# Optimization experiments

Measured on AMD Instinct MI355X. Metric: run time of the kernel, lower is better.

Reference implementation:

```python
import jax, jax.numpy as jnp
import numpy as np

N_NODES = 100000
N_EDGES = 3200000
_EPS = 1e-6

# SE3 layout: [tx, ty, tz, qx, qy, qz, qw] (pypose convention)

def _normalize_se3(T):
    t, q = T[..., :3], T[..., 3:7]
    q = q / jnp.linalg.norm(q, axis=-1, keepdims=True)
    return jnp.concatenate([t, q], axis=-1)

def _qmul(q, r):
    qx, qy, qz, qw = q[..., 0], q[..., 1], q[..., 2], q[..., 3]
    rx, ry, rz, rw = r[..., 0], r[..., 1], r[..., 2], r[..., 3]
    x = qw * rx + qx * rw + qy * rz - qz * ry
    y = qw * ry - qx * rz + qy * rw + qz * rx
    z = qw * rz + qx * ry - qy * rx + qz * rw
    w = qw * rw - qx * rx - qy * ry - qz * rz
    return jnp.stack([x, y, z, w], axis=-1)

def _qrot(q, v):
    # rotate vector v by unit quaternion q: v + 2 w (u x v) + 2 u x (u x v)
    u, w = q[..., :3], q[..., 3:4]
    t = 2.0 * jnp.cross(u, v)
    return v + w * t + jnp.cross(u, t)

def _se3_inv(T):
    t, q = T[..., :3], T[..., 3:7]
    qc = q * jnp.asarray([-1.0, -1.0, -1.0, 1.0], dtype=T.dtype)
    ti = -_qrot(qc, t)
    return jnp.concatenate([ti, qc], axis=-1)

def _se3_mul(A, B):
    ta, qa = A[..., :3], A[..., 3:7]
    tb, qb = B[..., :3], B[..., 3:7]
    return jnp.concatenate([ta + _qrot(qa, tb), _qmul(qa, qb)], axis=-1)

def _so3_log(q):
    # quaternion (xyzw) -> axis-angle 3-vector
    v, w = q[..., :3], q[..., 3]
    n = jnp.linalg.norm(v, axis=-1)
    n_safe = jnp.where(n > _EPS, n, 1.0)
    scale = jnp.where(n > _EPS, 2.0 * jnp.arctan2(n, w) / n_safe, 2.0 / jnp.where(jnp.abs(w) > _EPS, w, 1.0))
    return v * scale[..., None]

def _se3_log(T):
    # SE3 -> se3 = [tau(3), phi(3)], tau = Jl(phi)^{-1} t
    t, q = T[..., :3], T[..., 3:7]
    phi = _so3_log(q)
    theta = jnp.linalg.norm(phi, axis=-1)
    small = theta < _EPS
    th = jnp.where(small, 1.0, theta)
    c = jnp.where(small, 1.0 / 12.0, 1.0 / th**2 - (1.0 + jnp.cos(th)) / (2.0 * th * jnp.sin(th)))
    pxt = jnp.cross(phi, t)
    tau = t - 0.5 * pxt + c[..., None] * jnp.cross(phi, pxt)
    return jnp.concatenate([tau, phi], axis=-1)

def setup_inputs() -> dict:
    key = jax.random.key(0)
    k1, k2, k3 = jax.random.split(key, 3)
    nodes = _normalize_se3(jax.random.normal(k1, (N_NODES, 7), dtype=jnp.float32))
    poses = _normalize_se3(jax.random.normal(k2, (N_EDGES, 7), dtype=jnp.float32))
    edges = jax.random.randint(k3, (N_EDGES, 2), 0, N_NODES, dtype=jnp.int64)
    return {"edges": edges, "poses": poses, "nodes": nodes}

def reference(edges, poses, nodes):
    node1 = nodes[edges[..., 0]]  # [E, 7]
    node2 = nodes[edges[..., 1]]  # [E, 7]
    error = _se3_mul(_se3_mul(_se3_inv(poses), node2), _se3_inv(node1))
    return _se3_log(error)  # [E, 6]
```

## Files before the change

### kernel.cpp

```cpp
#include <hip/hip_runtime.h>
#include <math.h>

#define BLOCK 256
#define EPS 1e-6f


struct F3 { float x, y, z; };
struct F4 { float x, y, z, w; };

__device__ __forceinline__ F3 cross3(F3 a, F3 b) {
    return F3{a.y * b.z - a.z * b.y,
              a.z * b.x - a.x * b.z,
              a.x * b.y - a.y * b.x};
}
__device__ __forceinline__ F3 add3(F3 a, F3 b) { return F3{a.x + b.x, a.y + b.y, a.z + b.z}; }
__device__ __forceinline__ F3 neg3(F3 a) { return F3{-a.x, -a.y, -a.z}; }

__device__ __forceinline__ F3 qrot(F4 q, F3 v) {
    F3 u{q.x, q.y, q.z};
    F3 t = cross3(u, v);
    t.x *= 2.0f; t.y *= 2.0f; t.z *= 2.0f;
    F3 c = cross3(u, t);
    return F3{v.x + q.w * t.x + c.x,
              v.y + q.w * t.y + c.y,
              v.z + q.w * t.z + c.z};
}
__device__ __forceinline__ F4 qmul(F4 q, F4 r) {
    return F4{
        q.w * r.x + q.x * r.w + q.y * r.z - q.z * r.y,
        q.w * r.y - q.x * r.z + q.y * r.w + q.z * r.x,
        q.w * r.z + q.x * r.y - q.y * r.x + q.z * r.w,
        q.w * r.w - q.x * r.x - q.y * r.y - q.z * r.z};
}

__device__ __forceinline__ void se3_error_log(
    F3 tp, F4 qp, F3 t1, F4 q1, F3 t2, F4 q2, float o[6])
{
    F4 qpc{-qp.x, -qp.y, -qp.z, qp.w};
    F3 tpi = neg3(qrot(qpc, tp));

    F3 tA = add3(tpi, qrot(qpc, t2));
    F4 qA = qmul(qpc, q2);

    F4 q1c{-q1.x, -q1.y, -q1.z, q1.w};
    F3 t1i = neg3(qrot(q1c, t1));

    F3 tE = add3(tA, qrot(qA, t1i));
    F4 qE = qmul(qA, q1c);

    F3 v{qE.x, qE.y, qE.z};
    float w = qE.w;
    float nn = sqrtf(v.x * v.x + v.y * v.y + v.z * v.z);

    float scale, c;
    if (nn > EPS) {
        float ang = 2.0f * atan2f(nn, w);
        float u = 1.0f / (ang * nn);
        scale = u * ang * ang;
        c = u * (u * nn * nn - 0.5f * w);
    } else {
        scale = 2.0f / ((fabsf(w) > EPS) ? w : 1.0f);
        c = 1.0f / 12.0f;
    }

    F3 phi{v.x * scale, v.y * scale, v.z * scale};
    F3 pxt = cross3(phi, tE);
    F3 ppxt = cross3(phi, pxt);
    o[0] = tE.x - 0.5f * pxt.x + c * ppxt.x;
    o[1] = tE.y - 0.5f * pxt.y + c * ppxt.y;
    o[2] = tE.z - 0.5f * pxt.z + c * ppxt.z;
    o[3] = phi.x; o[4] = phi.y; o[5] = phi.z;
}

__device__ __forceinline__ void gload_lds16(const void* g, void* lds) {
    __builtin_amdgcn_global_load_lds(
        (const __attribute__((address_space(1))) void*)g,
        (__attribute__((address_space(3))) void*)lds,
        16, 0, 0);
}

__global__ void __launch_bounds__(BLOCK) repack_nodes_kernel(
    const float* __restrict__ nodes, float* __restrict__ nodes8, int total7)
{
    int idx = blockIdx.x * BLOCK + threadIdx.x;
    int stride = gridDim.x * BLOCK;
    for (; idx < total7; idx += stride) {
        int node = idx / 7;
        int comp = idx - node * 7;
        nodes8[node * 8 + comp] = nodes[idx];
    }
}

__global__ void __launch_bounds__(BLOCK) pose_graph_kernel(
    const int* __restrict__ edges,
    const float* __restrict__ poses,
    const float* __restrict__ nodes8,
    float* __restrict__ out,
    int n)
{
    __shared__ float4 G[4][256];

    const int tid = threadIdx.x;
    const int l = tid & 63;
    const int w = tid >> 6;
    const long long base = (long long)blockIdx.x * BLOCK;
    const int limit = (int)min((long long)BLOCK, (long long)n - base);

    if (limit == BLOCK) {
        const long long e = base + tid;

        float pa[4], pb[4];
        {
            const char* pp = (const char*)poses + (size_t)e * 28;
            __builtin_memcpy(pa, pp, 16);
            __builtin_memcpy(pb, pp + 12, 16);
        }

        const int2 ed = ((const int2*)edges)[e];

#pragma unroll
        for (int k = 0; k < 4; ++k) {
            const int o = k * 16 + (l >> 2);
            const int m = (l & 3) ^ ((o >> 1) & 3);
            const int nx = __shfl(ed.x, o, 64);
            const int ny = __shfl(ed.y, o, 64);
            const int idx = (m & 2) ? ny : nx;
            gload_lds16((const char*)nodes8 + ((size_t)idx * 32 + (size_t)(m & 1) * 16),
                        &G[w][k * 64]);
        }

        asm volatile("s_waitcnt vmcnt(0)" ::: "memory");

        const int xo = (l >> 1) & 3;
        const int b4 = l * 4;
        float4 a1 = G[w][b4 + (0 ^ xo)];
        float4 b1 = G[w][b4 + (1 ^ xo)];
        float4 a2 = G[w][b4 + (2 ^ xo)];
        float4 b2 = G[w][b4 + (3 ^ xo)];

        F3 tp{pa[0], pa[1], pa[2]};
        F4 qp{pb[0], pb[1], pb[2], pb[3]};
        F3 t1{a1.x, a1.y, a1.z};
        F4 q1{a1.w, b1.x, b1.y, b1.z};
        F3 t2{a2.x, a2.y, a2.z};
        F4 q2{a2.w, b2.x, b2.y, b2.z};

        float o6[6];
        se3_error_log(tp, qp, t1, q1, t2, q2, o6);

        float* Gf = (float*)&G[w][0];
        Gf[l * 6 + 0] = o6[0];
        Gf[l * 6 + 1] = o6[1];
        Gf[l * 6 + 2] = o6[2];
        Gf[l * 6 + 3] = o6[3];
        Gf[l * 6 + 4] = o6[4];
        Gf[l * 6 + 5] = o6[5];
        asm volatile("s_waitcnt lgkmcnt(0)" ::: "memory");

        float4* odst = (float4*)(out + base * 6);
        odst[w * 96 + l] = G[w][l];
        if (l < 32)
            odst[w * 96 + 64 + l] = G[w][64 + l];
    } else {
        if (tid < limit) {
            const long long e = base + tid;
            const int2 ed = ((const int2*)edges)[e];
            const float* pp = poses + e * 7;
            F3 tp{pp[0], pp[1], pp[2]};
            F4 qp{pp[3], pp[4], pp[5], pp[6]};
            const float4* n1p = (const float4*)(nodes8 + (size_t)ed.x * 8);
            const float4* n2p = (const float4*)(nodes8 + (size_t)ed.y * 8);
            float4 a1 = n1p[0], b1 = n1p[1];
            float4 a2 = n2p[0], b2 = n2p[1];
            F3 t1{a1.x, a1.y, a1.z};
            F4 q1{a1.w, b1.x, b1.y, b1.z};
            F3 t2{a2.x, a2.y, a2.z};
            F4 q2{a2.w, b2.x, b2.y, b2.z};
            float o6[6];
            se3_error_log(tp, qp, t1, q1, t2, q2, o6);
            float* op = out + e * 6;
            op[0] = o6[0]; op[1] = o6[1]; op[2] = o6[2];
            op[3] = o6[3]; op[4] = o6[4]; op[5] = o6[5];
        }
    }
}

__global__ void __launch_bounds__(BLOCK) pose_graph_kernel_fallback(
    const int* __restrict__ edges, const float* __restrict__ poses,
    const float* __restrict__ nodes, float* __restrict__ out, int n)
{
    const int tid = threadIdx.x;
    const long long base = (long long)blockIdx.x * BLOCK;
    const int limit = (int)min((long long)BLOCK, (long long)n - base);
    if (tid < limit) {
        const long long e = base + tid;
        const int2 ed = ((const int2*)edges)[e];
        const float* pp = poses + e * 7;
        F3 tp{pp[0], pp[1], pp[2]};
        F4 qp{pp[3], pp[4], pp[5], pp[6]};
        const float* n1p = nodes + (size_t)ed.x * 7;
        const float* n2p = nodes + (size_t)ed.y * 7;
        F3 t1{n1p[0], n1p[1], n1p[2]};
        F4 q1{n1p[3], n1p[4], n1p[5], n1p[6]};
        F3 t2{n2p[0], n2p[1], n2p[2]};
        F4 q2{n2p[3], n2p[4], n2p[5], n2p[6]};
        float o6[6];
        se3_error_log(tp, qp, t1, q1, t2, q2, o6);
        float* op = out + e * 6;
        op[0] = o6[0]; op[1] = o6[1]; op[2] = o6[2];
        op[3] = o6[3]; op[4] = o6[4]; op[5] = o6[5];
    }
}

extern "C" void kernel_launch(void* const* d_in, const int* in_sizes, int n_in,
                              void* d_out, int out_size, void* d_ws, size_t ws_size,
                              hipStream_t stream) {
    const int* edges = (const int*)d_in[0];
    const float* poses = (const float*)d_in[1];
    const float* nodes = (const float*)d_in[2];
    float* out = (float*)d_out;

    const int n_edges = in_sizes[0] / 2;
    const int n_nodes = in_sizes[2] / 7;
    const int grid = (n_edges + BLOCK - 1) / BLOCK;

    const size_t ws_needed = (size_t)n_nodes * 8 * sizeof(float);
    if (ws_size >= ws_needed) {
        float* nodes8 = (float*)d_ws;
        const int total7 = n_nodes * 7;
        const int rgrid = (total7 + BLOCK - 1) / BLOCK;
        repack_nodes_kernel<<<rgrid, BLOCK, 0, stream>>>(nodes, nodes8, total7);
        pose_graph_kernel<<<grid, BLOCK, 0, stream>>>(edges, poses, nodes8, out, n_edges);
    } else {
        pose_graph_kernel_fallback<<<grid, BLOCK, 0, stream>>>(edges, poses, nodes, out, n_edges);
    }
}
```

Before: 217.5 us.

## Process four edge chunks per thread with software-pipelined direct node loads

```diff
diff --git a/kernel.cpp b/kernel.cpp
--- a/kernel.cpp
+++ b/kernel.cpp
@@ -2,6 +2,8 @@
 #include <math.h>
 
 #define BLOCK 256
+#define CPT 4
+#define TILE (BLOCK * CPT)
 #define EPS 1e-6f
 
 
@@ -72,13 +74,6 @@
     o[3] = phi.x; o[4] = phi.y; o[5] = phi.z;
 }
 
-__device__ __forceinline__ void gload_lds16(const void* g, void* lds) {
-    __builtin_amdgcn_global_load_lds(
-        (const __attribute__((address_space(1))) void*)g,
-        (__attribute__((address_space(3))) void*)lds,
-        16, 0, 0);
-}
-
 __global__ void __launch_bounds__(BLOCK) repack_nodes_kernel(
     const float* __restrict__ nodes, float* __restrict__ nodes8, int total7)
 {
@@ -91,6 +86,54 @@
     }
 }
 
+__device__ __forceinline__ void load_nodes(
+    const float* __restrict__ nodes8, int2 ed,
+    float4& a1, float4& b1, float4& a2, float4& b2)
+{
+    const float4* n1p = (const float4*)(nodes8 + (size_t)ed.x * 8);
+    const float4* n2p = (const float4*)(nodes8 + (size_t)ed.y * 8);
+    a1 = n1p[0]; b1 = n1p[1];
+    a2 = n2p[0]; b2 = n2p[1];
+}
+
+__device__ __forceinline__ void load_pose(
+    const float* __restrict__ poses, long long e, float pa[4], float pb[4])
+{
+    const char* pp = (const char*)poses + (size_t)e * 28;
+    __builtin_memcpy(pa, pp, 16);
+    __builtin_memcpy(pb, pp + 12, 16);
+}
+
+__device__ __forceinline__ void compute_store(
+    const float pa[4], const float pb[4],
+    float4 a1, float4 b1, float4 a2, float4 b2,
+    float* __restrict__ so,
+    const float4* __restrict__ SOw,
+    float4* __restrict__ odst_j,
+    int l)
+{
+    F3 tp{pa[0], pa[1], pa[2]};
+    F4 qp{pb[0], pb[1], pb[2], pb[3]};
+    F3 t1{a1.x, a1.y, a1.z};
+    F4 q1{a1.w, b1.x, b1.y, b1.z};
+    F3 t2{a2.x, a2.y, a2.z};
+    F4 q2{a2.w, b2.x, b2.y, b2.z};
+
+    float o6[6];
+    se3_error_log(tp, qp, t1, q1, t2, q2, o6);
+
+    so[l * 6 + 0] = o6[0];
+    so[l * 6 + 1] = o6[1];
+    so[l * 6 + 2] = o6[2];
+    so[l * 6 + 3] = o6[3];
+    so[l * 6 + 4] = o6[4];
+    so[l * 6 + 5] = o6[5];
+    asm volatile("s_waitcnt lgkmcnt(0)" ::: "memory");
+
+    odst_j[l] = SOw[l];
+    if (l < 32) odst_j[64 + l] = SOw[64 + l];
+}
+
 __global__ void __launch_bounds__(BLOCK) pose_graph_kernel(
     const int* __restrict__ edges,
     const float* __restrict__ poses,
@@ -98,89 +141,64 @@
     float* __restrict__ out,
     int n)
 {
-    __shared__ float4 G[4][256];
+    __shared__ float4 SO[4][96];
 
     const int tid = threadIdx.x;
     const int l = tid & 63;
     const int w = tid >> 6;
-    const long long base = (long long)blockIdx.x * BLOCK;
-    const int limit = (int)min((long long)BLOCK, (long long)n - base);
-
-    if (limit == BLOCK) {
-        const long long e = base + tid;
-
-        float pa[4], pb[4];
-        {
-            const char* pp = (const char*)poses + (size_t)e * 28;
-            __builtin_memcpy(pa, pp, 16);
-            __builtin_memcpy(pb, pp + 12, 16);
-        }
-
-        const int2 ed = ((const int2*)edges)[e];
-
-#pragma unroll
-        for (int k = 0; k < 4; ++k) {
-            const int o = k * 16 + (l >> 2);
-            const int m = (l & 3) ^ ((o >> 1) & 3);
-            const int nx = __shfl(ed.x, o, 64);
-            const int ny = __shfl(ed.y, o, 64);
-            const int idx = (m & 2) ? ny : nx;
-            gload_lds16((const char*)nodes8 + ((size_t)idx * 32 + (size_t)(m & 1) * 16),
-                        &G[w][k * 64]);
-        }
-
-        asm volatile("s_waitcnt vmcnt(0)" ::: "memory");
-
-        const int xo = (l >> 1) & 3;
-        const int b4 = l * 4;
-        float4 a1 = G[w][b4 + (0 ^ xo)];
-        float4 b1 = G[w][b4 + (1 ^ xo)];
-        float4 a2 = G[w][b4 + (2 ^ xo)];
-        float4 b2 = G[w][b4 + (3 ^ xo)];
-
-        F3 tp{pa[0], pa[1], pa[2]};
-        F4 qp{pb[0], pb[1], pb[2], pb[3]};
-        F3 t1{a1.x, a1.y, a1.z};
-        F4 q1{a1.w, b1.x, b1.y, b1.z};
-        F3 t2{a2.x, a2.y, a2.z};
-        F4 q2{a2.w, b2.x, b2.y, b2.z};
-
-        float o6[6];
-        se3_error_log(tp, qp, t1, q1, t2, q2, o6);
-
-        float* Gf = (float*)&G[w][0];
-        Gf[l * 6 + 0] = o6[0];
-        Gf[l * 6 + 1] = o6[1];
-        Gf[l * 6 + 2] = o6[2];
-        Gf[l * 6 + 3] = o6[3];
-        Gf[l * 6 + 4] = o6[4];
-        Gf[l * 6 + 5] = o6[5];
-        asm volatile("s_waitcnt lgkmcnt(0)" ::: "memory");
-
+    const long long base = (long long)blockIdx.x * TILE;
+
+    if (base + TILE <= (long long)n) {
+        const long long e0 = base + tid;
+
+        int2 ed0 = ((const int2*)edges)[e0];
+        int2 ed1 = ((const int2*)edges)[e0 + BLOCK];
+        int2 ed2 = ((const int2*)edges)[e0 + 2 * BLOCK];
+        int2 ed3 = ((const int2*)edges)[e0 + 3 * BLOCK];
+
+        float* so = (float*)&SO[w][0];
+        const float4* SOw = &SO[w][0];
         float4* odst = (float4*)(out + base * 6);
-        odst[w * 96 + l] = G[w][l];
-        if (l < 32)
-            odst[w * 96 + 64 + l] = G[w][64 + l];
+
+        float4 Aa, Ab, Ac, Ad; float Apa[4], Apb[4];
+        float4 Ba, Bb, Bc, Bd; float Bpa[4], Bpb[4];
+
+        load_nodes(nodes8, ed0, Aa, Ab, Ac, Ad);
+        load_pose(poses, e0, Apa, Apb);
+        load_nodes(nodes8, ed1, Ba, Bb, Bc, Bd);
+        load_pose(poses, e0 + BLOCK, Bpa, Bpb);
+
+        compute_store(Apa, Apb, Aa, Ab, Ac, Ad, so, SOw, odst + 0 * 384 + w * 96, l);
+        load_nodes(nodes8, ed2, Aa, Ab, Ac, Ad);
+        load_pose(poses, e0 + 2 * BLOCK, Apa, Apb);
+
+        compute_store(Bpa, Bpb, Ba, Bb, Bc, Bd, so, SOw, odst + 1 * 384 + w * 96, l);
+        load_nodes(nodes8, ed3, Ba, Bb, Bc, Bd);
+        load_pose(poses, e0 + 3 * BLOCK, Bpa, Bpb);
+
+        compute_store(Apa, Apb, Aa, Ab, Ac, Ad, so, SOw, odst + 2 * 384 + w * 96, l);
+        compute_store(Bpa, Bpb, Ba, Bb, Bc, Bd, so, SOw, odst + 3 * 384 + w * 96, l);
     } else {
-        if (tid < limit) {
-            const long long e = base + tid;
-            const int2 ed = ((const int2*)edges)[e];
-            const float* pp = poses + e * 7;
-            F3 tp{pp[0], pp[1], pp[2]};
-            F4 qp{pp[3], pp[4], pp[5], pp[6]};
-            const float4* n1p = (const float4*)(nodes8 + (size_t)ed.x * 8);
-            const float4* n2p = (const float4*)(nodes8 + (size_t)ed.y * 8);
-            float4 a1 = n1p[0], b1 = n1p[1];
-            float4 a2 = n2p[0], b2 = n2p[1];
-            F3 t1{a1.x, a1.y, a1.z};
-            F4 q1{a1.w, b1.x, b1.y, b1.z};
-            F3 t2{a2.x, a2.y, a2.z};
-            F4 q2{a2.w, b2.x, b2.y, b2.z};
-            float o6[6];
-            se3_error_log(tp, qp, t1, q1, t2, q2, o6);
-            float* op = out + e * 6;
-            op[0] = o6[0]; op[1] = o6[1]; op[2] = o6[2];
-            op[3] = o6[3]; op[4] = o6[4]; op[5] = o6[5];
+        for (int j = 0; j < CPT; ++j) {
+            const long long e = base + j * BLOCK + tid;
+            if (e < (long long)n) {
+                const int2 ed = ((const int2*)edges)[e];
+                float pa[4], pb[4];
+                load_pose(poses, e, pa, pb);
+                float4 a1, b1, a2, b2;
+                load_nodes(nodes8, ed, a1, b1, a2, b2);
+                F3 tp{pa[0], pa[1], pa[2]};
+                F4 qp{pb[0], pb[1], pb[2], pb[3]};
+                F3 t1{a1.x, a1.y, a1.z};
+                F4 q1{a1.w, b1.x, b1.y, b1.z};
+                F3 t2{a2.x, a2.y, a2.z};
+                F4 q2{a2.w, b2.x, b2.y, b2.z};
+                float o6[6];
+                se3_error_log(tp, qp, t1, q1, t2, q2, o6);
+                float* op = out + e * 6;
+                op[0] = o6[0]; op[1] = o6[1]; op[2] = o6[2];
+                op[3] = o6[3]; op[4] = o6[4]; op[5] = o6[5];
+            }
         }
     }
 }
@@ -222,16 +240,17 @@
 
     const int n_edges = in_sizes[0] / 2;
     const int n_nodes = in_sizes[2] / 7;
-    const int grid = (n_edges + BLOCK - 1) / BLOCK;
 
     const size_t ws_needed = (size_t)n_nodes * 8 * sizeof(float);
     if (ws_size >= ws_needed) {
         float* nodes8 = (float*)d_ws;
         const int total7 = n_nodes * 7;
         const int rgrid = (total7 + BLOCK - 1) / BLOCK;
+        const int grid = (n_edges + TILE - 1) / TILE;
         repack_nodes_kernel<<<rgrid, BLOCK, 0, stream>>>(nodes, nodes8, total7);
         pose_graph_kernel<<<grid, BLOCK, 0, stream>>>(edges, poses, nodes8, out, n_edges);
     } else {
+        const int grid = (n_edges + BLOCK - 1) / BLOCK;
         pose_graph_kernel_fallback<<<grid, BLOCK, 0, stream>>>(edges, poses, nodes, out, n_edges);
     }
 }
```

New measurement: 239.2 us. 1.1x slower.

## Process four edge chunks per block with double-buffered LDS gathers

Applied to the files above, without the earlier changes.

```diff
diff --git a/kernel.cpp b/kernel.cpp
--- a/kernel.cpp
+++ b/kernel.cpp
@@ -2,6 +2,8 @@
 #include <math.h>
 
 #define BLOCK 256
+#define CPT 4
+#define TILE (BLOCK * CPT)
 #define EPS 1e-6f
 
 
@@ -79,6 +81,65 @@
         16, 0, 0);
 }
 
+__device__ __forceinline__ void gather_wave(
+    const float* __restrict__ nodes8, int2 ed, int l, float4* __restrict__ GW)
+{
+#pragma unroll
+    for (int k = 0; k < 4; ++k) {
+        const int o = k * 16 + (l >> 2);
+        const int m = (l & 3) ^ ((o >> 1) & 3);
+        const int nx = __shfl(ed.x, o, 64);
+        const int ny = __shfl(ed.y, o, 64);
+        const int idx = (m & 2) ? ny : nx;
+        gload_lds16((const char*)nodes8 + ((size_t)idx * 32 + (size_t)(m & 1) * 16),
+                    GW + k * 64);
+    }
+}
+
+__device__ __forceinline__ void load_pose(
+    const float* __restrict__ poses, long long e, float pa[4], float pb[4])
+{
+    const char* pp = (const char*)poses + (size_t)e * 28;
+    __builtin_memcpy(pa, pp, 16);
+    __builtin_memcpy(pb, pp + 12, 16);
+}
+
+__device__ __forceinline__ void compute_store(
+    const float pa[4], const float pb[4],
+    float4* __restrict__ GW,
+    float4* __restrict__ odst_j,
+    int l)
+{
+    const int xo = (l >> 1) & 3;
+    const int b4 = l * 4;
+    float4 a1 = GW[b4 + (0 ^ xo)];
+    float4 b1 = GW[b4 + (1 ^ xo)];
+    float4 a2 = GW[b4 + (2 ^ xo)];
+    float4 b2 = GW[b4 + (3 ^ xo)];
+
+    F3 tp{pa[0], pa[1], pa[2]};
+    F4 qp{pb[0], pb[1], pb[2], pb[3]};
+    F3 t1{a1.x, a1.y, a1.z};
+    F4 q1{a1.w, b1.x, b1.y, b1.z};
+    F3 t2{a2.x, a2.y, a2.z};
+    F4 q2{a2.w, b2.x, b2.y, b2.z};
+
+    float o6[6];
+    se3_error_log(tp, qp, t1, q1, t2, q2, o6);
+
+    float* Gf = (float*)GW;
+    Gf[l * 6 + 0] = o6[0];
+    Gf[l * 6 + 1] = o6[1];
+    Gf[l * 6 + 2] = o6[2];
+    Gf[l * 6 + 3] = o6[3];
+    Gf[l * 6 + 4] = o6[4];
+    Gf[l * 6 + 5] = o6[5];
+    asm volatile("s_waitcnt lgkmcnt(0)" ::: "memory");
+
+    odst_j[l] = GW[l];
+    if (l < 32) odst_j[64 + l] = GW[64 + l];
+}
+
 __global__ void __launch_bounds__(BLOCK) repack_nodes_kernel(
     const float* __restrict__ nodes, float* __restrict__ nodes8, int total7)
 {
@@ -98,89 +159,74 @@
     float* __restrict__ out,
     int n)
 {
-    __shared__ float4 G[4][256];
+    __shared__ float4 G[4][2][256];
 
     const int tid = threadIdx.x;
     const int l = tid & 63;
     const int w = tid >> 6;
-    const long long base = (long long)blockIdx.x * BLOCK;
-    const int limit = (int)min((long long)BLOCK, (long long)n - base);
-
-    if (limit == BLOCK) {
-        const long long e = base + tid;
-
-        float pa[4], pb[4];
-        {
-            const char* pp = (const char*)poses + (size_t)e * 28;
-            __builtin_memcpy(pa, pp, 16);
-            __builtin_memcpy(pb, pp + 12, 16);
-        }
-
-        const int2 ed = ((const int2*)edges)[e];
-
-#pragma unroll
-        for (int k = 0; k < 4; ++k) {
-            const int o = k * 16 + (l >> 2);
-            const int m = (l & 3) ^ ((o >> 1) & 3);
-            const int nx = __shfl(ed.x, o, 64);
-            const int ny = __shfl(ed.y, o, 64);
-            const int idx = (m & 2) ? ny : nx;
-            gload_lds16((const char*)nodes8 + ((size_t)idx * 32 + (size_t)(m & 1) * 16),
-                        &G[w][k * 64]);
-        }
+    const long long base = (long long)blockIdx.x * TILE;
+
+    if (base + TILE <= (long long)n) {
+        const long long e0 = base + tid;
+
+        const int2 ed0 = ((const int2*)edges)[e0];
+        const int2 ed1 = ((const int2*)edges)[e0 + BLOCK];
+        const int2 ed2 = ((const int2*)edges)[e0 + 2 * BLOCK];
+        const int2 ed3 = ((const int2*)edges)[e0 + 3 * BLOCK];
+
+        float4* odst = (float4*)(out + base * 6);
+        float4* B0 = &G[w][0][0];
+        float4* B1 = &G[w][1][0];
+
+        float pa0[4], pb0[4], pa1[4], pb1[4];
+
+        gather_wave(nodes8, ed0, l, B0);
+        load_pose(poses, e0, pa0, pb0);
+
+        gather_wave(nodes8, ed1, l, B1);
+        load_pose(poses, e0 + BLOCK, pa1, pb1);
+        asm volatile("s_waitcnt vmcnt(8)" ::: "memory");
+        __builtin_amdgcn_sched_barrier(0);
+        compute_store(pa0, pb0, B0, odst + 0 * 384 + w * 96, l);
+
+        gather_wave(nodes8, ed2, l, B0);
+        load_pose(poses, e0 + 2 * BLOCK, pa0, pb0);
+        asm volatile("s_waitcnt vmcnt(8)" ::: "memory");
+        __builtin_amdgcn_sched_barrier(0);
+        compute_store(pa1, pb1, B1, odst + 1 * 384 + w * 96, l);
+
+        gather_wave(nodes8, ed3, l, B1);
+        load_pose(poses, e0 + 3 * BLOCK, pa1, pb1);
+        asm volatile("s_waitcnt vmcnt(8)" ::: "memory");
+        __builtin_amdgcn_sched_barrier(0);
+        compute_store(pa0, pb0, B0, odst + 2 * 384 + w * 96, l);
 
         asm volatile("s_waitcnt vmcnt(0)" ::: "memory");
-
-        const int xo = (l >> 1) & 3;
-        const int b4 = l * 4;
-        float4 a1 = G[w][b4 + (0 ^ xo)];
-        float4 b1 = G[w][b4 + (1 ^ xo)];
-        float4 a2 = G[w][b4 + (2 ^ xo)];
-        float4 b2 = G[w][b4 + (3 ^ xo)];
-
-        F3 tp{pa[0], pa[1], pa[2]};
-        F4 qp{pb[0], pb[1], pb[2], pb[3]};
-        F3 t1{a1.x, a1.y, a1.z};
-        F4 q1{a1.w, b1.x, b1.y, b1.z};
-        F3 t2{a2.x, a2.y, a2.z};
-        F4 q2{a2.w, b2.x, b2.y, b2.z};
-
-        float o6[6];
-        se3_error_log(tp, qp, t1, q1, t2, q2, o6);
-
-        float* Gf = (float*)&G[w][0];
-        Gf[l * 6 + 0] = o6[0];
-        Gf[l * 6 + 1] = o6[1];
-        Gf[l * 6 + 2] = o6[2];
-        Gf[l * 6 + 3] = o6[3];
-        Gf[l * 6 + 4] = o6[4];
-        Gf[l * 6 + 5] = o6[5];
-        asm volatile("s_waitcnt lgkmcnt(0)" ::: "memory");
-
-        float4* odst = (float4*)(out + base * 6);
-        odst[w * 96 + l] = G[w][l];
-        if (l < 32)
-            odst[w * 96 + 64 + l] = G[w][64 + l];
+        __builtin_amdgcn_sched_barrier(0);
+        compute_store(pa1, pb1, B1, odst + 3 * 384 + w * 96, l);
     } else {
-        if (tid < limit) {
-            const long long e = base + tid;
-            const int2 ed = ((const int2*)edges)[e];
-            const float* pp = poses + e * 7;
-            F3 tp{pp[0], pp[1], pp[2]};
-            F4 qp{pp[3], pp[4], pp[5], pp[6]};
-            const float4* n1p = (const float4*)(nodes8 + (size_t)ed.x * 8);
-            const float4* n2p = (const float4*)(nodes8 + (size_t)ed.y * 8);
-            float4 a1 = n1p[0], b1 = n1p[1];
-            float4 a2 = n2p[0], b2 = n2p[1];
-            F3 t1{a1.x, a1.y, a1.z};
-            F4 q1{a1.w, b1.x, b1.y, b1.z};
-            F3 t2{a2.x, a2.y, a2.z};
-            F4 q2{a2.w, b2.x, b2.y, b2.z};
-            float o6[6];
-            se3_error_log(tp, qp, t1, q1, t2, q2, o6);
-            float* op = out + e * 6;
-            op[0] = o6[0]; op[1] = o6[1]; op[2] = o6[2];
-            op[3] = o6[3]; op[4] = o6[4]; op[5] = o6[5];
+        for (int j = 0; j < CPT; ++j) {
+            const long long e = base + j * BLOCK + tid;
+            if (e < (long long)n) {
+                const int2 ed = ((const int2*)edges)[e];
+                float pa[4], pb[4];
+                load_pose(poses, e, pa, pb);
+                const float4* n1p = (const float4*)(nodes8 + (size_t)ed.x * 8);
+                const float4* n2p = (const float4*)(nodes8 + (size_t)ed.y * 8);
+                float4 a1 = n1p[0], b1 = n1p[1];
+                float4 a2 = n2p[0], b2 = n2p[1];
+                F3 tp{pa[0], pa[1], pa[2]};
+                F4 qp{pb[0], pb[1], pb[2], pb[3]};
+                F3 t1{a1.x, a1.y, a1.z};
+                F4 q1{a1.w, b1.x, b1.y, b1.z};
+                F3 t2{a2.x, a2.y, a2.z};
+                F4 q2{a2.w, b2.x, b2.y, b2.z};
+                float o6[6];
+                se3_error_log(tp, qp, t1, q1, t2, q2, o6);
+                float* op = out + e * 6;
+                op[0] = o6[0]; op[1] = o6[1]; op[2] = o6[2];
+                op[3] = o6[3]; op[4] = o6[4]; op[5] = o6[5];
+            }
         }
     }
 }
@@ -222,16 +268,17 @@
 
     const int n_edges = in_sizes[0] / 2;
     const int n_nodes = in_sizes[2] / 7;
-    const int grid = (n_edges + BLOCK - 1) / BLOCK;
 
     const size_t ws_needed = (size_t)n_nodes * 8 * sizeof(float);
     if (ws_size >= ws_needed) {
         float* nodes8 = (float*)d_ws;
         const int total7 = n_nodes * 7;
         const int rgrid = (total7 + BLOCK - 1) / BLOCK;
+        const int grid = (n_edges + TILE - 1) / TILE;
         repack_nodes_kernel<<<rgrid, BLOCK, 0, stream>>>(nodes, nodes8, total7);
         pose_graph_kernel<<<grid, BLOCK, 0, stream>>>(edges, poses, nodes8, out, n_edges);
     } else {
+        const int grid = (n_edges + BLOCK - 1) / BLOCK;
         pose_graph_kernel_fallback<<<grid, BLOCK, 0, stream>>>(edges, poses, nodes, out, n_edges);
     }
 }
```

Measured after the change: 218.7 us. About the same (+0.5%).
